# Kernel tuning notes

Measured on AMD Instinct MI355X. Metric: run time of the kernel, lower is better.

The kernel has to match this reference:

```python
import jax, jax.numpy as jnp
import numpy as np

EPS = 1e-08

def quantize_weights(w):
    # absmean ternary quantization: round(w/delta) clipped to {-1,0,1}, rescaled by delta
    delta = jnp.mean(jnp.abs(w)) + EPS
    w_quant = jnp.clip(jnp.round(w / delta), -1.0, 1.0)
    return w_quant * delta

def setup_inputs() -> dict:
    key = jax.random.key(0)
    k1, k2 = jax.random.split(key)
    B, T, IN, OUT = 8, 16, 4096, 11008
    x = jax.random.normal(k1, (B, T, IN), dtype=jnp.float32)
    weight = jax.random.normal(k2, (OUT, IN), dtype=jnp.float32)
    bias = jnp.zeros((OUT,), dtype=jnp.float32)
    return {"x": x, "weight": weight, "bias": bias}

def reference(x, weight, bias):
    w_quant = quantize_weights(weight)
    # F.linear: x @ w_quant.T + bias
    out = jnp.einsum("bti,oi->bto", x, w_quant) + bias
    return out
```

## Files before the change

kernel.cpp:

```cpp
#include <hip/hip_runtime.h>
#include <hip/hip_bf16.h>

typedef __bf16 bf16x8 __attribute__((ext_vector_type(8)));
typedef float f32x4 __attribute__((ext_vector_type(4)));
typedef unsigned short ushort8 __attribute__((ext_vector_type(8)));
typedef unsigned short ushort4v __attribute__((ext_vector_type(4)));

constexpr int M = 128;
constexpr int K = 4096;
constexpr int N = 11008;
constexpr int BN = 128;
constexpr int BK = 32;
constexpr int KSPLIT = 8;
constexpr long long NW = (long long)N * K;
constexpr int RBLK = 2048;

constexpr size_t PART_OFF = 0;
constexpr size_t XBF_OFF  = 8192;
constexpr size_t P_OFF    = XBF_OFF + (size_t)M * K * 2;
constexpr size_t MN       = (size_t)M * N;
constexpr size_t WS_NEED  = P_OFF + KSPLIT * MN * sizeof(float);

__device__ __forceinline__ unsigned short f2bf_bits(float f) {
    unsigned int u = __builtin_bit_cast(unsigned int, f);
    u += 0x7FFFu + ((u >> 16) & 1u);
    return (unsigned short)(u >> 16);
}

template <bool CVT>
__global__ __launch_bounds__(256) void absmean_partial(const float* __restrict__ w,
                                                       const float* __restrict__ x,
                                                       float* __restrict__ partials,
                                                       unsigned short* __restrict__ xbf)
{
    const int gtid = blockIdx.x * blockDim.x + threadIdx.x;
    if (CVT && gtid < M * K / 8) {
        const float4* xp = (const float4*)x + (size_t)gtid * 2;
        float4 a = xp[0], b = xp[1];
        ushort8 o;
        o[0] = f2bf_bits(a.x); o[1] = f2bf_bits(a.y);
        o[2] = f2bf_bits(a.z); o[3] = f2bf_bits(a.w);
        o[4] = f2bf_bits(b.x); o[5] = f2bf_bits(b.y);
        o[6] = f2bf_bits(b.z); o[7] = f2bf_bits(b.w);
        *(ushort8*)(xbf + (size_t)gtid * 8) = o;
    }
    const int n4 = (int)(NW / 4);
    const float4* w4 = (const float4*)w;
    float s0 = 0.f, s1 = 0.f, s2 = 0.f, s3 = 0.f;
    for (int i = gtid; i < n4; i += gridDim.x * blockDim.x) {
        float4 v = w4[i];
        s0 += fabsf(v.x); s1 += fabsf(v.y); s2 += fabsf(v.z); s3 += fabsf(v.w);
    }
    float s = (s0 + s1) + (s2 + s3);
#pragma unroll
    for (int off = 32; off > 0; off >>= 1) s += __shfl_down(s, off, 64);
    __shared__ float red[4];
    if ((threadIdx.x & 63) == 0) red[threadIdx.x >> 6] = s;
    __syncthreads();
    if (threadIdx.x == 0)
        partials[blockIdx.x] = (red[0] + red[1]) + (red[2] + red[3]);
}

template <int KSTEPS, bool PRE>
__global__ __launch_bounds__(256, 3) void bitlinear_gemm(
    const void* __restrict__ Xsrc, const float* __restrict__ W,
    const float* __restrict__ bias, const float* __restrict__ partials,
    float* __restrict__ dbase)
{
    constexpr int LDSW = 40;
    __shared__ __attribute__((aligned(16))) unsigned short xs[2][M * LDSW];
    __shared__ __attribute__((aligned(16))) unsigned short wsm[2][BN * LDSW];

    const int tid = threadIdx.x;
    const int lane = tid & 63;
    const int wid = tid >> 6;
    const int wm = wid >> 1;
    const int wn = wid & 1;
    const int cgrp = lane >> 4;
    const int l15 = lane & 15;
    const int n0 = blockIdx.x * BN;
    const int kk0 = PRE ? blockIdx.y * (K / KSPLIT) : 0;
    const int K4 = K / 4;

    const unsigned short* xb = (const unsigned short*)Xsrc;
    const float4* xf = (const float4*)Xsrc;
    const float4* w4p = (const float4*)W;

    ushort8 xr[2];
    float4 wr[4];

    auto issue = [&](int t) {
#pragma unroll
        for (int i = 0; i < 2; ++i) {
            const int j = tid + i * 256;
            const int row = j >> 2, ch = j & 3;
            if (PRE) {
                xr[i] = *(const ushort8*)(xb + (size_t)row * K + kk0 + t * BK + ch * 8);
            } else {
                const float4* xp = xf + (size_t)row * K4 + t * (BK / 4) + ch * 2;
                float4 a = xp[0], b = xp[1];
                ushort8 o;
                o[0] = f2bf_bits(a.x); o[1] = f2bf_bits(a.y);
                o[2] = f2bf_bits(a.z); o[3] = f2bf_bits(a.w);
                o[4] = f2bf_bits(b.x); o[5] = f2bf_bits(b.y);
                o[6] = f2bf_bits(b.z); o[7] = f2bf_bits(b.w);
                xr[i] = o;
            }
        }
#pragma unroll
        for (int i = 0; i < 4; ++i) {
            const int j = tid + i * 256;
            const int row = j >> 3, q = j & 7;
            wr[i] = w4p[(size_t)(n0 + row) * K4 + kk0 / 4 + t * (BK / 4) + q];
        }
    };

    issue(0);

    float s = 0.f;
#pragma unroll
    for (int i = 0; i < RBLK / 256; ++i) s += partials[tid + i * 256];
#pragma unroll
    for (int off = 32; off > 0; off >>= 1) s += __shfl_down(s, off, 64);
    __shared__ float red[4];
    if (lane == 0) red[wid] = s;
    __syncthreads();
    const float delta =
        (float)((double)((red[0] + red[1]) + (red[2] + red[3])) / (double)NW + 1e-8);
    const float inv_delta = 1.0f / delta;

    auto stage = [&](int buf) {
#pragma unroll
        for (int i = 0; i < 2; ++i) {
            const int j = tid + i * 256;
            *(ushort8*)&xs[buf][(j >> 2) * LDSW + (j & 3) * 8] = xr[i];
        }
#pragma unroll
        for (int i = 0; i < 4; ++i) {
            const int j = tid + i * 256;
            const int row = j >> 3, q = j & 7;
            float wf[4] = {wr[i].x, wr[i].y, wr[i].z, wr[i].w};
            ushort4v wq;
#pragma unroll
            for (int e = 0; e < 4; ++e) {
                float qv = rintf(wf[e] * inv_delta);
                qv = fminf(1.f, fmaxf(-1.f, qv));
                wq[e] = f2bf_bits(qv);
            }
            *(ushort4v*)&wsm[buf][row * LDSW + q * 4] = wq;
        }
    };

    stage(0);
    __syncthreads();

    f32x4 acc[4][4] = {};

    for (int t = 0; t < KSTEPS; ++t) {
        const int cur = t & 1;
        if (t + 1 < KSTEPS) issue(t + 1);
        const unsigned short* xcur = xs[cur];
        const unsigned short* wcur = wsm[cur];
        bf16x8 afr[4], bfr[4];
#pragma unroll
        for (int f = 0; f < 4; ++f)
            afr[f] = *(const bf16x8*)&xcur[(wm * 64 + f * 16 + l15) * LDSW + cgrp * 8];
#pragma unroll
        for (int g = 0; g < 4; ++g)
            bfr[g] = *(const bf16x8*)&wcur[(wn * 64 + g * 16 + l15) * LDSW + cgrp * 8];
#pragma unroll
        for (int f = 0; f < 4; ++f)
#pragma unroll
            for (int g = 0; g < 4; ++g)
                acc[f][g] = __builtin_amdgcn_mfma_f32_16x16x32_bf16(
                    afr[f], bfr[g], acc[f][g], 0, 0, 0);
        if (t + 1 < KSTEPS) stage(cur ^ 1);
        __syncthreads();
    }

    float* dst = PRE ? dbase + (size_t)blockIdx.y * MN : dbase;
#pragma unroll
    for (int f = 0; f < 4; ++f) {
        const int mrow = wm * 64 + f * 16 + cgrp * 4;
#pragma unroll
        for (int g = 0; g < 4; ++g) {
            const int ocol = n0 + wn * 64 + g * 16 + l15;
            const float bv = PRE ? 0.f : bias[ocol];
#pragma unroll
            for (int r = 0; r < 4; ++r)
                dst[(size_t)(mrow + r) * N + ocol] = delta * acc[f][g][r] + bv;
        }
    }
}

__global__ __launch_bounds__(256) void combine(const float* __restrict__ p,
                                               const float* __restrict__ bias,
                                               float4* __restrict__ out)
{
    const int i4 = blockIdx.x * blockDim.x + threadIdx.x;
    constexpr int N4 = N / 4;
    if (i4 >= (int)(MN / 4)) return;
    const int col4 = i4 % N4;
    float4 s = *(const float4*)(bias + col4 * 4);
#pragma unroll
    for (int y = 0; y < KSPLIT; ++y) {
        float4 v = ((const float4*)(p + y * MN))[i4];
        s.x += v.x; s.y += v.y; s.z += v.z; s.w += v.w;
    }
    out[i4] = s;
}

extern "C" void kernel_launch(void* const* d_in, const int* in_sizes, int n_in,
                              void* d_out, int out_size, void* d_ws, size_t ws_size,
                              hipStream_t stream) {
    const float* x = (const float*)d_in[0];
    const float* w = (const float*)d_in[1];
    const float* bias = (const float*)d_in[2];
    float* out = (float*)d_out;
    float* partials = (float*)((char*)d_ws + PART_OFF);
    unsigned short* xbf = (unsigned short*)((char*)d_ws + XBF_OFF);
    float* pbase = (float*)((char*)d_ws + P_OFF);

    if (ws_size >= WS_NEED) {
        absmean_partial<true><<<RBLK, 256, 0, stream>>>(w, x, partials, xbf);
        bitlinear_gemm<K / KSPLIT / BK, true><<<dim3(N / BN, KSPLIT), 256, 0, stream>>>(
            xbf, w, bias, partials, pbase);
        combine<<<(int)(MN / 4 + 255) / 256, 256, 0, stream>>>(pbase, bias, (float4*)out);
    } else {
        absmean_partial<false><<<RBLK, 256, 0, stream>>>(w, x, partials, xbf);
        bitlinear_gemm<K / BK, false><<<dim3(N / BN, 1), 256, 0, stream>>>(
            x, w, bias, partials, out);
    }
}
```

Baseline: 77.32 us.

## Fuse absmean reduction into GEMM via cooperative grid sync, halve K-split

```diff
diff --git a/kernel.cpp b/kernel.cpp
--- a/kernel.cpp
+++ b/kernel.cpp
@@ -1,5 +1,8 @@
 #include <hip/hip_runtime.h>
 #include <hip/hip_bf16.h>
+#include <hip/hip_cooperative_groups.h>
+
+namespace cg = cooperative_groups;
 
 typedef __bf16 bf16x8 __attribute__((ext_vector_type(8)));
 typedef float f32x4 __attribute__((ext_vector_type(4)));
@@ -11,15 +14,17 @@
 constexpr int N = 11008;
 constexpr int BN = 128;
 constexpr int BK = 32;
-constexpr int KSPLIT = 8;
+constexpr int KSPLIT = 4;
+constexpr int KBLK = K / KSPLIT;
+constexpr int NBX = N / BN;
+constexpr int GRID = NBX * KSPLIT;
 constexpr long long NW = (long long)N * K;
-constexpr int RBLK = 2048;
+constexpr size_t MN = (size_t)M * N;
 
 constexpr size_t PART_OFF = 0;
-constexpr size_t XBF_OFF  = 8192;
-constexpr size_t P_OFF    = XBF_OFF + (size_t)M * K * 2;
-constexpr size_t MN       = (size_t)M * N;
-constexpr size_t WS_NEED  = P_OFF + KSPLIT * MN * sizeof(float);
+constexpr size_t P_OFF = 8192;
+constexpr size_t WS_NEED_SPLIT = P_OFF + KSPLIT * MN * sizeof(float);
+constexpr size_t WS_NEED_MIN = GRID * sizeof(float);
 
 __device__ __forceinline__ unsigned short f2bf_bits(float f) {
     unsigned int u = __builtin_bit_cast(unsigned int, f);
@@ -27,49 +32,39 @@
     return (unsigned short)(u >> 16);
 }
 
-template <bool CVT>
-__global__ __launch_bounds__(256) void absmean_partial(const float* __restrict__ w,
-                                                       const float* __restrict__ x,
-                                                       float* __restrict__ partials,
-                                                       unsigned short* __restrict__ xbf)
+__global__ __launch_bounds__(256) void absmean_tiles(const float* __restrict__ W,
+                                                     float* __restrict__ partials)
 {
-    const int gtid = blockIdx.x * blockDim.x + threadIdx.x;
-    if (CVT && gtid < M * K / 8) {
-        const float4* xp = (const float4*)x + (size_t)gtid * 2;
-        float4 a = xp[0], b = xp[1];
-        ushort8 o;
-        o[0] = f2bf_bits(a.x); o[1] = f2bf_bits(a.y);
-        o[2] = f2bf_bits(a.z); o[3] = f2bf_bits(a.w);
-        o[4] = f2bf_bits(b.x); o[5] = f2bf_bits(b.y);
-        o[6] = f2bf_bits(b.z); o[7] = f2bf_bits(b.w);
-        *(ushort8*)(xbf + (size_t)gtid * 8) = o;
-    }
-    const int n4 = (int)(NW / 4);
-    const float4* w4 = (const float4*)w;
+    const int tid = threadIdx.x;
+    const int n0 = blockIdx.x * BN, kk0 = blockIdx.y * KBLK;
+    const float4* w4p = (const float4*)W;
+    const int K4 = K / 4;
     float s0 = 0.f, s1 = 0.f, s2 = 0.f, s3 = 0.f;
-    for (int i = gtid; i < n4; i += gridDim.x * blockDim.x) {
-        float4 v = w4[i];
+    for (int r = 0; r < BN; ++r) {
+        float4 v = w4p[(size_t)(n0 + r) * K4 + kk0 / 4 + tid];
         s0 += fabsf(v.x); s1 += fabsf(v.y); s2 += fabsf(v.z); s3 += fabsf(v.w);
     }
     float s = (s0 + s1) + (s2 + s3);
 #pragma unroll
     for (int off = 32; off > 0; off >>= 1) s += __shfl_down(s, off, 64);
     __shared__ float red[4];
-    if ((threadIdx.x & 63) == 0) red[threadIdx.x >> 6] = s;
+    if ((tid & 63) == 0) red[tid >> 6] = s;
     __syncthreads();
-    if (threadIdx.x == 0)
-        partials[blockIdx.x] = (red[0] + red[1]) + (red[2] + red[3]);
-}
-
-template <int KSTEPS, bool PRE>
-__global__ __launch_bounds__(256, 3) void bitlinear_gemm(
-    const void* __restrict__ Xsrc, const float* __restrict__ W,
-    const float* __restrict__ bias, const float* __restrict__ partials,
+    if (tid == 0)
+        partials[blockIdx.y * NBX + blockIdx.x] = (red[0] + red[1]) + (red[2] + red[3]);
+}
+
+template <bool COOP, bool DIRECT>
+__global__ __launch_bounds__(256, 2) void bitlinear_fused(
+    const float* __restrict__ X, const float* __restrict__ W,
+    const float* __restrict__ bias, float* __restrict__ partials,
     float* __restrict__ dbase)
 {
+    constexpr int KSTEPS = DIRECT ? K / BK : KBLK / BK;
     constexpr int LDSW = 40;
     __shared__ __attribute__((aligned(16))) unsigned short xs[2][M * LDSW];
     __shared__ __attribute__((aligned(16))) unsigned short wsm[2][BN * LDSW];
+    __shared__ float red[4];
 
     const int tid = threadIdx.x;
     const int lane = tid & 63;
@@ -79,54 +74,66 @@
     const int cgrp = lane >> 4;
     const int l15 = lane & 15;
     const int n0 = blockIdx.x * BN;
-    const int kk0 = PRE ? blockIdx.y * (K / KSPLIT) : 0;
+    const int by = DIRECT ? 0 : blockIdx.y;
+    const int kk0 = DIRECT ? 0 : by * KBLK;
     const int K4 = K / 4;
-
-    const unsigned short* xb = (const unsigned short*)Xsrc;
-    const float4* xf = (const float4*)Xsrc;
     const float4* w4p = (const float4*)W;
+    const float4* x4p = (const float4*)X;
+
+    if constexpr (COOP) {
+        float s0 = 0.f, s1 = 0.f, s2 = 0.f, s3 = 0.f;
+        for (int r = 0; r < BN; ++r) {
+            float4 v = w4p[(size_t)(n0 + r) * K4 + kk0 / 4 + tid];
+            s0 += fabsf(v.x); s1 += fabsf(v.y); s2 += fabsf(v.z); s3 += fabsf(v.w);
+        }
+        float s = (s0 + s1) + (s2 + s3);
+#pragma unroll
+        for (int off = 32; off > 0; off >>= 1) s += __shfl_down(s, off, 64);
+        if (lane == 0) red[wid] = s;
+        __syncthreads();
+        if (tid == 0)
+            partials[by * NBX + blockIdx.x] = (red[0] + red[1]) + (red[2] + red[3]);
+        cg::this_grid().sync();
+    }
 
     ushort8 xr[2];
-    float4 wr[4];
+    float4 wrf[4];
 
     auto issue = [&](int t) {
 #pragma unroll
         for (int i = 0; i < 2; ++i) {
             const int j = tid + i * 256;
             const int row = j >> 2, ch = j & 3;
-            if (PRE) {
-                xr[i] = *(const ushort8*)(xb + (size_t)row * K + kk0 + t * BK + ch * 8);
-            } else {
-                const float4* xp = xf + (size_t)row * K4 + t * (BK / 4) + ch * 2;
-                float4 a = xp[0], b = xp[1];
-                ushort8 o;
-                o[0] = f2bf_bits(a.x); o[1] = f2bf_bits(a.y);
-                o[2] = f2bf_bits(a.z); o[3] = f2bf_bits(a.w);
-                o[4] = f2bf_bits(b.x); o[5] = f2bf_bits(b.y);
-                o[6] = f2bf_bits(b.z); o[7] = f2bf_bits(b.w);
-                xr[i] = o;
-            }
+            const float4* xp = x4p + (size_t)row * K4 + (kk0 + t * BK) / 4 + ch * 2;
+            float4 a = xp[0], b = xp[1];
+            ushort8 o;
+            o[0] = f2bf_bits(a.x); o[1] = f2bf_bits(a.y);
+            o[2] = f2bf_bits(a.z); o[3] = f2bf_bits(a.w);
+            o[4] = f2bf_bits(b.x); o[5] = f2bf_bits(b.y);
+            o[6] = f2bf_bits(b.z); o[7] = f2bf_bits(b.w);
+            xr[i] = o;
         }
 #pragma unroll
         for (int i = 0; i < 4; ++i) {
             const int j = tid + i * 256;
             const int row = j >> 3, q = j & 7;
-            wr[i] = w4p[(size_t)(n0 + row) * K4 + kk0 / 4 + t * (BK / 4) + q];
+            wrf[i] = w4p[(size_t)(n0 + row) * K4 + (kk0 + t * BK) / 4 + q];
         }
     };
 
     issue(0);
 
-    float s = 0.f;
-#pragma unroll
-    for (int i = 0; i < RBLK / 256; ++i) s += partials[tid + i * 256];
-#pragma unroll
-    for (int off = 32; off > 0; off >>= 1) s += __shfl_down(s, off, 64);
-    __shared__ float red[4];
-    if (lane == 0) red[wid] = s;
-    __syncthreads();
-    const float delta =
-        (float)((double)((red[0] + red[1]) + (red[2] + red[3])) / (double)NW + 1e-8);
+    float delta;
+    {
+        float s = 0.f;
+        for (int i = tid; i < GRID; i += 256) s += partials[i];
+#pragma unroll
+        for (int off = 32; off > 0; off >>= 1) s += __shfl_down(s, off, 64);
+        if (lane == 0) red[wid] = s;
+        __syncthreads();
+        delta = (float)((double)((red[0] + red[1]) + (red[2] + red[3])) /
+                        (double)NW + 1e-8);
+    }
     const float inv_delta = 1.0f / delta;
 
     auto stage = [&](int buf) {
@@ -139,7 +146,7 @@
         for (int i = 0; i < 4; ++i) {
             const int j = tid + i * 256;
             const int row = j >> 3, q = j & 7;
-            float wf[4] = {wr[i].x, wr[i].y, wr[i].z, wr[i].w};
+            float wf[4] = {wrf[i].x, wrf[i].y, wrf[i].z, wrf[i].w};
             ushort4v wq;
 #pragma unroll
             for (int e = 0; e < 4; ++e) {
@@ -178,14 +185,14 @@
         __syncthreads();
     }
 
-    float* dst = PRE ? dbase + (size_t)blockIdx.y * MN : dbase;
+    float* dst = DIRECT ? dbase : dbase + (size_t)by * MN;
 #pragma unroll
     for (int f = 0; f < 4; ++f) {
         const int mrow = wm * 64 + f * 16 + cgrp * 4;
 #pragma unroll
         for (int g = 0; g < 4; ++g) {
             const int ocol = n0 + wn * 64 + g * 16 + l15;
-            const float bv = PRE ? 0.f : bias[ocol];
+            const float bv = DIRECT ? bias[ocol] : 0.f;
 #pragma unroll
             for (int r = 0; r < 4; ++r)
                 dst[(size_t)(mrow + r) * N + ocol] = delta * acc[f][g][r] + bv;
@@ -218,17 +225,23 @@
     const float* bias = (const float*)d_in[2];
     float* out = (float*)d_out;
     float* partials = (float*)((char*)d_ws + PART_OFF);
-    unsigned short* xbf = (unsigned short*)((char*)d_ws + XBF_OFF);
     float* pbase = (float*)((char*)d_ws + P_OFF);
 
-    if (ws_size >= WS_NEED) {
-        absmean_partial<true><<<RBLK, 256, 0, stream>>>(w, x, partials, xbf);
-        bitlinear_gemm<K / KSPLIT / BK, true><<<dim3(N / BN, KSPLIT), 256, 0, stream>>>(
-            xbf, w, bias, partials, pbase);
+    if (ws_size >= WS_NEED_SPLIT) {
+        const void* kf = reinterpret_cast<const void*>(&bitlinear_fused<true, false>);
+        void* kargs[] = {(void*)&x, (void*)&w, (void*)&bias,
+                         (void*)&partials, (void*)&pbase};
+        hipError_t rc = hipLaunchCooperativeKernel(kf, dim3(NBX, KSPLIT), dim3(256),
+                                                   kargs, 0, stream);
+        if (rc != hipSuccess) {
+            absmean_tiles<<<dim3(NBX, KSPLIT), 256, 0, stream>>>(w, partials);
+            bitlinear_fused<false, false><<<dim3(NBX, KSPLIT), 256, 0, stream>>>(
+                x, w, bias, partials, pbase);
+        }
         combine<<<(int)(MN / 4 + 255) / 256, 256, 0, stream>>>(pbase, bias, (float4*)out);
-    } else {
-        absmean_partial<false><<<RBLK, 256, 0, stream>>>(w, x, partials, xbf);
-        bitlinear_gemm<K / BK, false><<<dim3(N / BN, 1), 256, 0, stream>>>(
+    } else if (ws_size >= WS_NEED_MIN) {
+        absmean_tiles<<<dim3(NBX, KSPLIT), 256, 0, stream>>>(w, partials);
+        bitlinear_fused<false, true><<<dim3(NBX, 1), 256, 0, stream>>>(
             x, w, bias, partials, out);
     }
 }
```

New measurement: 140.1 us. 1.81x slower.

## Halve GEMM tile width and KSPLIT, add two-deep register prefetch pipeline

Applied to the files above, without the earlier changes.

```diff
diff --git a/kernel.cpp b/kernel.cpp
--- a/kernel.cpp
+++ b/kernel.cpp
@@ -9,17 +9,20 @@
 constexpr int M = 128;
 constexpr int K = 4096;
 constexpr int N = 11008;
-constexpr int BN = 128;
+constexpr int BN = 64;
 constexpr int BK = 32;
-constexpr int KSPLIT = 8;
+constexpr int KSPLIT = 4;
+constexpr int KBLK = K / KSPLIT;
+constexpr int NBX = N / BN;
 constexpr long long NW = (long long)N * K;
 constexpr int RBLK = 2048;
+constexpr size_t MN = (size_t)M * N;
 
 constexpr size_t PART_OFF = 0;
 constexpr size_t XBF_OFF  = 8192;
 constexpr size_t P_OFF    = XBF_OFF + (size_t)M * K * 2;
-constexpr size_t MN       = (size_t)M * N;
 constexpr size_t WS_NEED  = P_OFF + KSPLIT * MN * sizeof(float);
+constexpr size_t WS_MIN   = RBLK * sizeof(float);
 
 __device__ __forceinline__ unsigned short f2bf_bits(float f) {
     unsigned int u = __builtin_bit_cast(unsigned int, f);
@@ -62,7 +65,7 @@
 }
 
 template <int KSTEPS, bool PRE>
-__global__ __launch_bounds__(256, 3) void bitlinear_gemm(
+__global__ __launch_bounds__(256, 4) void bitlinear_gemm(
     const void* __restrict__ Xsrc, const float* __restrict__ W,
     const float* __restrict__ bias, const float* __restrict__ partials,
     float* __restrict__ dbase)
@@ -70,6 +73,7 @@
     constexpr int LDSW = 40;
     __shared__ __attribute__((aligned(16))) unsigned short xs[2][M * LDSW];
     __shared__ __attribute__((aligned(16))) unsigned short wsm[2][BN * LDSW];
+    __shared__ float red[4];
 
     const int tid = threadIdx.x;
     const int lane = tid & 63;
@@ -79,66 +83,77 @@
     const int cgrp = lane >> 4;
     const int l15 = lane & 15;
     const int n0 = blockIdx.x * BN;
-    const int kk0 = PRE ? blockIdx.y * (K / KSPLIT) : 0;
+    const int kk0 = PRE ? blockIdx.y * KBLK : 0;
     const int K4 = K / 4;
 
     const unsigned short* xb = (const unsigned short*)Xsrc;
-    const float4* xf = (const float4*)Xsrc;
+    const float4* x4p = (const float4*)Xsrc;
     const float4* w4p = (const float4*)W;
 
-    ushort8 xr[2];
-    float4 wr[4];
-
-    auto issue = [&](int t) {
+    ushort8 xrA[2], xrB[2];
+    float4 xfA[4], xfB[4];
+    float4 wrA[2], wrB[2];
+
+    auto issue_set = [&](int t, ushort8 (&xr)[2], float4 (&xf)[4], float4 (&wr)[2]) {
+        if constexpr (PRE) {
+#pragma unroll
+            for (int i = 0; i < 2; ++i) {
+                const int j = tid + i * 256;
+                xr[i] = *(const ushort8*)(xb + (size_t)(j >> 2) * K + kk0 + t * BK + (j & 3) * 8);
+            }
+        } else {
+#pragma unroll
+            for (int i = 0; i < 4; ++i) {
+                const int j = tid + i * 256;
+                xf[i] = x4p[(size_t)(j >> 3) * K4 + (t * BK) / 4 + (j & 7)];
+            }
+        }
 #pragma unroll
         for (int i = 0; i < 2; ++i) {
             const int j = tid + i * 256;
-            const int row = j >> 2, ch = j & 3;
-            if (PRE) {
-                xr[i] = *(const ushort8*)(xb + (size_t)row * K + kk0 + t * BK + ch * 8);
-            } else {
-                const float4* xp = xf + (size_t)row * K4 + t * (BK / 4) + ch * 2;
-                float4 a = xp[0], b = xp[1];
-                ushort8 o;
-                o[0] = f2bf_bits(a.x); o[1] = f2bf_bits(a.y);
-                o[2] = f2bf_bits(a.z); o[3] = f2bf_bits(a.w);
-                o[4] = f2bf_bits(b.x); o[5] = f2bf_bits(b.y);
-                o[6] = f2bf_bits(b.z); o[7] = f2bf_bits(b.w);
-                xr[i] = o;
-            }
-        }
-#pragma unroll
-        for (int i = 0; i < 4; ++i) {
-            const int j = tid + i * 256;
-            const int row = j >> 3, q = j & 7;
-            wr[i] = w4p[(size_t)(n0 + row) * K4 + kk0 / 4 + t * (BK / 4) + q];
+            wr[i] = w4p[(size_t)(n0 + (j >> 3)) * K4 + (kk0 + t * BK) / 4 + (j & 7)];
         }
     };
 
-    issue(0);
+    float ps[RBLK / 256];
+#pragma unroll
+    for (int i = 0; i < RBLK / 256; ++i) ps[i] = partials[tid + i * 256];
+
+    issue_set(0, xrA, xfA, wrA);
+    if (KSTEPS > 1) issue_set(1, xrB, xfB, wrB);
 
     float s = 0.f;
 #pragma unroll
-    for (int i = 0; i < RBLK / 256; ++i) s += partials[tid + i * 256];
+    for (int i = 0; i < RBLK / 256; ++i) s += ps[i];
 #pragma unroll
     for (int off = 32; off > 0; off >>= 1) s += __shfl_down(s, off, 64);
-    __shared__ float red[4];
     if (lane == 0) red[wid] = s;
     __syncthreads();
     const float delta =
         (float)((double)((red[0] + red[1]) + (red[2] + red[3])) / (double)NW + 1e-8);
     const float inv_delta = 1.0f / delta;
 
-    auto stage = [&](int buf) {
+    auto stage_set = [&](int buf, ushort8 (&xr)[2], float4 (&xf)[4], float4 (&wr)[2]) {
+        if constexpr (PRE) {
+#pragma unroll
+            for (int i = 0; i < 2; ++i) {
+                const int j = tid + i * 256;
+                *(ushort8*)&xs[buf][(j >> 2) * LDSW + (j & 3) * 8] = xr[i];
+            }
+        } else {
+#pragma unroll
+            for (int i = 0; i < 4; ++i) {
+                const int j = tid + i * 256;
+                float4 v = xf[i];
+                ushort4v o;
+                o[0] = f2bf_bits(v.x); o[1] = f2bf_bits(v.y);
+                o[2] = f2bf_bits(v.z); o[3] = f2bf_bits(v.w);
+                *(ushort4v*)&xs[buf][(j >> 3) * LDSW + (j & 7) * 4] = o;
+            }
+        }
 #pragma unroll
         for (int i = 0; i < 2; ++i) {
             const int j = tid + i * 256;
-            *(ushort8*)&xs[buf][(j >> 2) * LDSW + (j & 3) * 8] = xr[i];
-        }
-#pragma unroll
-        for (int i = 0; i < 4; ++i) {
-            const int j = tid + i * 256;
-            const int row = j >> 3, q = j & 7;
             float wf[4] = {wr[i].x, wr[i].y, wr[i].z, wr[i].w};
             ushort4v wq;
 #pragma unroll
@@ -147,35 +162,39 @@
                 qv = fminf(1.f, fmaxf(-1.f, qv));
                 wq[e] = f2bf_bits(qv);
             }
-            *(ushort4v*)&wsm[buf][row * LDSW + q * 4] = wq;
+            *(ushort4v*)&wsm[buf][(j >> 3) * LDSW + (j & 7) * 4] = wq;
         }
     };
 
-    stage(0);
-    __syncthreads();
-
-    f32x4 acc[4][4] = {};
-
-    for (int t = 0; t < KSTEPS; ++t) {
-        const int cur = t & 1;
-        if (t + 1 < KSTEPS) issue(t + 1);
-        const unsigned short* xcur = xs[cur];
-        const unsigned short* wcur = wsm[cur];
-        bf16x8 afr[4], bfr[4];
+    f32x4 acc[4][2] = {};
+
+    auto compute = [&](int buf) {
+        const unsigned short* xcur = xs[buf];
+        const unsigned short* wcur = wsm[buf];
+        bf16x8 afr[4], bfr[2];
 #pragma unroll
         for (int f = 0; f < 4; ++f)
             afr[f] = *(const bf16x8*)&xcur[(wm * 64 + f * 16 + l15) * LDSW + cgrp * 8];
 #pragma unroll
-        for (int g = 0; g < 4; ++g)
-            bfr[g] = *(const bf16x8*)&wcur[(wn * 64 + g * 16 + l15) * LDSW + cgrp * 8];
+        for (int g = 0; g < 2; ++g)
+            bfr[g] = *(const bf16x8*)&wcur[(wn * 32 + g * 16 + l15) * LDSW + cgrp * 8];
 #pragma unroll
         for (int f = 0; f < 4; ++f)
 #pragma unroll
-            for (int g = 0; g < 4; ++g)
+            for (int g = 0; g < 2; ++g)
                 acc[f][g] = __builtin_amdgcn_mfma_f32_16x16x32_bf16(
                     afr[f], bfr[g], acc[f][g], 0, 0, 0);
-        if (t + 1 < KSTEPS) stage(cur ^ 1);
+    };
+
+    for (int t = 0; t < KSTEPS; t += 2) {
+        stage_set(0, xrA, xfA, wrA);
+        if (t + 2 < KSTEPS) issue_set(t + 2, xrA, xfA, wrA);
         __syncthreads();
+        compute(0);
+        stage_set(1, xrB, xfB, wrB);
+        if (t + 3 < KSTEPS) issue_set(t + 3, xrB, xfB, wrB);
+        __syncthreads();
+        compute(1);
     }
 
     float* dst = PRE ? dbase + (size_t)blockIdx.y * MN : dbase;
@@ -183,8 +202,8 @@
     for (int f = 0; f < 4; ++f) {
         const int mrow = wm * 64 + f * 16 + cgrp * 4;
 #pragma unroll
-        for (int g = 0; g < 4; ++g) {
-            const int ocol = n0 + wn * 64 + g * 16 + l15;
+        for (int g = 0; g < 2; ++g) {
+            const int ocol = n0 + wn * 32 + g * 16 + l15;
             const float bv = PRE ? 0.f : bias[ocol];
 #pragma unroll
             for (int r = 0; r < 4; ++r)
@@ -223,12 +242,12 @@
 
     if (ws_size >= WS_NEED) {
         absmean_partial<true><<<RBLK, 256, 0, stream>>>(w, x, partials, xbf);
-        bitlinear_gemm<K / KSPLIT / BK, true><<<dim3(N / BN, KSPLIT), 256, 0, stream>>>(
+        bitlinear_gemm<KBLK / BK, true><<<dim3(NBX, KSPLIT), 256, 0, stream>>>(
             xbf, w, bias, partials, pbase);
         combine<<<(int)(MN / 4 + 255) / 256, 256, 0, stream>>>(pbase, bias, (float4*)out);
-    } else {
+    } else if (ws_size >= WS_MIN) {
         absmean_partial<false><<<RBLK, 256, 0, stream>>>(w, x, partials, xbf);
-        bitlinear_gemm<K / BK, false><<<dim3(N / BN, 1), 256, 0, stream>>>(
+        bitlinear_gemm<K / BK, false><<<dim3(NBX, 1), 256, 0, stream>>>(
             x, w, bias, partials, out);
     }
 }
```

Result: faster. 71.67 us (-7.3%).
